# Kernel tuning notes

Measured on AMD Instinct MI355X. Metric: run time of the kernel, lower is better.

## Reference

```python
import jax, jax.numpy as jnp
import numpy as np

T, B, I, H = 512, 64, 1024, 1024


def setup_inputs() -> dict:
    key = jax.random.key(0)
    ks = jax.random.split(key, 7)
    k = 1.0 / np.sqrt(H)  # torch LSTM default init scale
    return {
        "x": jax.random.normal(ks[0], (T, B, I), dtype=jnp.float32),
        "h0": jax.random.normal(ks[1], (B, H), dtype=jnp.float32),
        "c0": jax.random.normal(ks[2], (B, H), dtype=jnp.float32),
        "W_ih": jax.random.uniform(ks[3], (4 * H, I), minval=-k, maxval=k, dtype=jnp.float32),
        "W_hh": jax.random.uniform(ks[4], (4 * H, H), minval=-k, maxval=k, dtype=jnp.float32),
        "b_ih": jax.random.uniform(ks[5], (4 * H,), minval=-k, maxval=k, dtype=jnp.float32),
        "b_hh": jax.random.uniform(ks[6], (4 * H,), minval=-k, maxval=k, dtype=jnp.float32),
    }


def reference(x, h0, c0, W_ih, W_hh, b_ih, b_hh):
    # Precompute input projections for all timesteps in one big GEMM: [T,B,4H]
    x_proj = jnp.einsum("tbi,gi->tbg", x, W_ih) + b_ih

    def step(carry, xg):
        h, c = carry
        gates = xg + h @ W_hh.T + b_hh  # [B, 4H]
        i_g, f_g, g_g, o_g = jnp.split(gates, 4, axis=-1)
        i_g = jax.nn.sigmoid(i_g)
        f_g = jax.nn.sigmoid(f_g)
        g_g = jnp.tanh(g_g)
        o_g = jax.nn.sigmoid(o_g)
        c = f_g * c + i_g * g_g
        h = o_g * jnp.tanh(c)
        return (h, c), h

    (hT, cT), outputs = jax.lax.scan(step, (h0, c0), x_proj)
    return outputs, hT, cT
```

## Files before the change

kernel.cpp:

```cpp
#include <hip/hip_runtime.h>


typedef __attribute__((ext_vector_type(8))) short bf16x8;
typedef __attribute__((ext_vector_type(4))) short bf16x4;
typedef __attribute__((ext_vector_type(4))) float f32x4;
typedef __attribute__((ext_vector_type(4))) unsigned int u32x4;
typedef unsigned long long u64;

#define T_STEPS 512
#define BATCH   64
#define HID     1024
#define G4      4096
#define BH      (BATCH * HID)
#define NSLOT   64

#define OFF_XPT   ((size_t)0)
#define OFF_RING  ((size_t)268435456)
#define OFF_WIB   ((size_t)335544320)
#define OFF_WHB   ((size_t)343932928)
#define OFF_BSUM  ((size_t)352321536)

__device__ __forceinline__ unsigned short f2bf(float f) {
  unsigned int u = __float_as_uint(f);
  u += 0x7FFFu + ((u >> 16) & 1u);
  return (unsigned short)(u >> 16);
}
__device__ __forceinline__ float bf2f(short s) {
  return __uint_as_float(((unsigned int)(unsigned short)s) << 16);
}
__device__ __forceinline__ float sigm(float x) { return 1.0f / (1.0f + __expf(-x)); }
__device__ __forceinline__ float tanh_f(float x) {
  float e = __expf(-2.0f * fabsf(x));
  float r = (1.0f - e) / (1.0f + e);
  return x < 0.0f ? -r : r;
}

__device__ __forceinline__ void gl_lds16(const unsigned short* g, unsigned short* l) {
  __builtin_amdgcn_global_load_lds(
      (const __attribute__((address_space(1))) unsigned int*)g,
      (__attribute__((address_space(3))) unsigned int*)l, 16, 0, 0);
}

__device__ __forceinline__ u32x4 llc_load4(const unsigned int* p) {
  u32x4 r;
  asm volatile("global_load_dwordx4 %0, %1, off sc0 sc1"
               : "=&v"(r) : "v"(p));
  return r;
}

__global__ void k_cast_bf16(const float* __restrict__ src,
                            unsigned short* __restrict__ dst, int n) {
  int i = (blockIdx.x * 256 + threadIdx.x) * 4;
  if (i >= n) return;
  float4 v = *(const float4*)(src + i);
  bf16x4 o;
  o[0] = (short)f2bf(v.x); o[1] = (short)f2bf(v.y);
  o[2] = (short)f2bf(v.z); o[3] = (short)f2bf(v.w);
  *(bf16x4*)(dst + i) = o;
}

__global__ void k_bias(const float* __restrict__ bi, const float* __restrict__ bh,
                       float* __restrict__ bs) {
  int i = blockIdx.x * 256 + threadIdx.x;
  if (i < G4) bs[i] = bi[i] + bh[i];
}

__global__ void k_h0_pack(const float* __restrict__ h0,
                          unsigned int* __restrict__ ring32) {
  int i = blockIdx.x * 256 + threadIdx.x;
  unsigned int pk = ((unsigned int)f2bf(h0[i]) << 16) | 1u;
  __hip_atomic_store(ring32 + i, pk, __ATOMIC_RELAXED, __HIP_MEMORY_SCOPE_AGENT);
}

__launch_bounds__(256, 2)
__global__ void k_xproj(const unsigned short* __restrict__ xb,
                        const unsigned short* __restrict__ wib,
                        const float* __restrict__ bs,
                        unsigned short* __restrict__ xpT) {
  __shared__ __align__(16) unsigned short ldsW[2][128 * 64];
  __shared__ __align__(16) unsigned short ldsX[2][128 * 64];

  const int tid  = threadIdx.x;
  const int lane = tid & 63;
  const int w    = tid >> 6;
  const int nt   = blockIdx.x & 31;
  const int mt   = blockIdx.x >> 5;
  const int n0   = nt * 128;
  const int m0   = mt * 128;
  const int col  = lane & 15;
  const int kq   = lane >> 4;

  const int srow = lane >> 3;
  const int swzu = (lane & 7) ^ srow;

  const unsigned short* wsrc = wib + (size_t)n0 * 1024;
  const unsigned short* xsrc = xb  + (size_t)m0 * 1024;

  const int wm = (w & 1) * 64;
  const int wn = (w >> 1) * 64;

  f32x4 acc[4][4];
#pragma unroll
  for (int i = 0; i < 4; ++i)
#pragma unroll
    for (int j = 0; j < 4; ++j) acc[i][j] = (f32x4){0.f, 0.f, 0.f, 0.f};

  auto STAGE = [&](int b, int kt) {
#pragma unroll
    for (int q = 0; q < 4; ++q) {
      const int rbase = q * 32 + w * 8;
      const size_t goff = (size_t)(rbase + srow) * 1024 + kt * 64 + swzu * 8;
      gl_lds16(wsrc + goff, &ldsW[b][rbase * 64]);
      gl_lds16(xsrc + goff, &ldsX[b][rbase * 64]);
    }
  };

  STAGE(0, 0);
  int buf = 0;
  for (int kt = 0; kt < 16; ++kt) {
    asm volatile("s_waitcnt vmcnt(0)" ::: "memory");
    __syncthreads();
    if (kt < 15) STAGE(buf ^ 1, kt + 1);
#pragma unroll
    for (int ks = 0; ks < 2; ++ks) {
      bf16x8 af[4], bfr[4];
#pragma unroll
      for (int mm = 0; mm < 4; ++mm) {
        const int row = wm + mm * 16 + col;
        const int un  = (ks * 4 + kq) ^ (row & 7);
        af[mm] = *(const bf16x8*)&ldsX[buf][row * 64 + un * 8];
      }
#pragma unroll
      for (int nn = 0; nn < 4; ++nn) {
        const int row = wn + nn * 16 + col;
        const int un  = (ks * 4 + kq) ^ (row & 7);
        bfr[nn] = *(const bf16x8*)&ldsW[buf][row * 64 + un * 8];
      }
#pragma unroll
      for (int mm = 0; mm < 4; ++mm)
#pragma unroll
        for (int nn = 0; nn < 4; ++nn)
          acc[mm][nn] = __builtin_amdgcn_mfma_f32_16x16x32_bf16(
              af[mm], bfr[nn], acc[mm][nn], 0, 0, 0);
    }
    __syncthreads();
    buf ^= 1;
  }

#pragma unroll
  for (int nn = 0; nn < 4; ++nn) {
    const int nrow = n0 + wn + nn * 16 + col;
    const float bias = bs[nrow];
#pragma unroll
    for (int mm = 0; mm < 4; ++mm) {
      bf16x4 ov;
#pragma unroll
      for (int r = 0; r < 4; ++r) ov[r] = (short)f2bf(acc[mm][nn][r] + bias);
      *(bf16x4*)(xpT + (size_t)nrow * 32768 + m0 + wm + mm * 16 + kq * 4) = ov;
    }
  }
}

__launch_bounds__(256, 1)
__global__ void k_lstm(const unsigned short* __restrict__ whb,
                       const unsigned short* __restrict__ xpT,
                       const float* __restrict__ c0,
                       unsigned int* __restrict__ ring32,
                       float* __restrict__ out) {
  const int tid  = threadIdx.x;
  const int lane = tid & 63;
  const int w    = tid >> 6;
  const int jsl  = blockIdx.x & 63;
  const int brow = blockIdx.x >> 6;
  const int b0   = brow * 16;
  const int j0   = jsl * 16;
  const int col  = lane & 15;
  const int kq   = lane >> 4;
  const int kch  = kq * 8;

  __shared__ __align__(16) unsigned char hbf[32 * 1024];
  __shared__ float glds[4][16][17];

  bf16x8 Wr[32];
  {
    const unsigned short* wp = whb + (size_t)(w * 1024 + j0 + col) * 1024 + kch;
#pragma unroll
    for (int s = 0; s < 32; ++s) Wr[s] = *(const bf16x8*)(wp + s * 32);
  }

  const int bl = tid >> 4, cc = tid & 15;
  float c = c0[(b0 + bl) * 1024 + j0 + cc];

  const unsigned short* xprow =
      xpT + (size_t)(w * 1024 + j0 + col) * 32768 + b0 + kq * 4;
  bf16x4 xv = *(const bf16x4*)(xprow);

  const size_t lrow = (size_t)(b0 + col) * 1024 + kq * 8;

  auto STAGE_H = [&](size_t slotbase, unsigned int tg) {
    const unsigned int* sb = ring32 + slotbase + lrow;
    u32x4 q0[8], q1[8];
#pragma unroll
    for (int i = 0; i < 8; ++i) {
      q0[i] = *(const u32x4*)(sb + (w * 8 + i) * 32);
      q1[i] = *(const u32x4*)(sb + (w * 8 + i) * 32 + 4);
    }
    unsigned int pend = 0xFFu;
    for (;;) {
#pragma unroll
      for (int i = 0; i < 8; ++i)
        if (pend & (1u << i)) {
          unsigned int bad =
              ((q0[i][0] ^ tg) | (q0[i][1] ^ tg) | (q0[i][2] ^ tg) | (q0[i][3] ^ tg) |
               (q1[i][0] ^ tg) | (q1[i][1] ^ tg) | (q1[i][2] ^ tg) | (q1[i][3] ^ tg)) &
              0xFFFFu;
          if (bad == 0u) {
            u32x4 o;
            o[0] = (q0[i][0] >> 16) | (q0[i][1] & 0xFFFF0000u);
            o[1] = (q0[i][2] >> 16) | (q0[i][3] & 0xFFFF0000u);
            o[2] = (q1[i][0] >> 16) | (q1[i][1] & 0xFFFF0000u);
            o[3] = (q1[i][2] >> 16) | (q1[i][3] & 0xFFFF0000u);
            *(u32x4*)(hbf + (w * 8 + i) * 1024 + lane * 16) = o;
            pend &= ~(1u << i);
          }
        }
      if (__all(pend == 0u)) break;
#pragma unroll
      for (int i = 0; i < 8; ++i)
        if (pend & (1u << i)) {
          q0[i] = llc_load4(sb + (w * 8 + i) * 32);
          q1[i] = llc_load4(sb + (w * 8 + i) * 32 + 4);
        }
      asm volatile("s_waitcnt vmcnt(0)" ::: "memory");
      __builtin_amdgcn_sched_barrier(0);
    }
  };

  STAGE_H(0, 1u);

  for (int t = 0; t < T_STEPS; ++t) {
    __syncthreads();

    f32x4 acc0 = (f32x4){0.f, 0.f, 0.f, 0.f};
    f32x4 acc1 = (f32x4){0.f, 0.f, 0.f, 0.f};
#pragma unroll
    for (int s = 0; s < 32; s += 2) {
      bf16x8 a0 = *(const bf16x8*)(hbf + s * 1024 + lane * 16);
      bf16x8 a1 = *(const bf16x8*)(hbf + (s + 1) * 1024 + lane * 16);
      acc0 = __builtin_amdgcn_mfma_f32_16x16x32_bf16(a0, Wr[s],     acc0, 0, 0, 0);
      acc1 = __builtin_amdgcn_mfma_f32_16x16x32_bf16(a1, Wr[s + 1], acc1, 0, 0, 0);
    }

#pragma unroll
    for (int r = 0; r < 4; ++r) {
      float v = (acc0[r] + acc1[r]) + bf2f(xv[r]);
      float g = (w == 2) ? tanh_f(v) : sigm(v);
      glds[w][kq * 4 + r][col] = g;
    }
    __syncthreads();

    float ig = glds[0][bl][cc], fg = glds[1][bl][cc];
    float gg = glds[2][bl][cc], og = glds[3][bl][cc];
    c = fg * c + ig * gg;
    float h = og * tanh_f(c);

    if (t < T_STEPS - 1) {
      unsigned int pk = ((unsigned int)f2bf(h) << 16) | (unsigned int)(t + 2);
      __hip_atomic_store(ring32 + (size_t)((t + 1) & (NSLOT - 1)) * BH +
                             (size_t)(b0 + bl) * 1024 + (j0 + cc),
                         pk, __ATOMIC_RELAXED, __HIP_MEMORY_SCOPE_AGENT);
    }

    const int hoff = (b0 + bl) * 1024 + j0 + cc;
    out[(size_t)t * BH + hoff] = h;
    if (t == T_STEPS - 1) {
      out[(size_t)T_STEPS * BH + hoff] = h;
      out[(size_t)T_STEPS * BH + BH + hoff] = c;
    } else {
      xv = *(const bf16x4*)(xprow + (size_t)(t + 1) * 64);
      STAGE_H((size_t)((t + 1) & (NSLOT - 1)) * BH, (unsigned int)(t + 2));
    }
  }
}

extern "C" void kernel_launch(void* const* d_in, const int* in_sizes, int n_in,
                              void* d_out, int out_size, void* d_ws, size_t ws_size,
                              hipStream_t stream) {
  const float* x   = (const float*)d_in[0];
  const float* h0  = (const float*)d_in[1];
  const float* c0  = (const float*)d_in[2];
  const float* Wih = (const float*)d_in[3];
  const float* Whh = (const float*)d_in[4];
  const float* bih = (const float*)d_in[5];
  const float* bhh = (const float*)d_in[6];
  float* out = (float*)d_out;
  char* ws = (char*)d_ws;

  unsigned short* xpT  = (unsigned short*)(ws + OFF_XPT);
  unsigned int*   ring = (unsigned int*)(ws + OFF_RING);
  unsigned short* wib  = (unsigned short*)(ws + OFF_WIB);
  unsigned short* whb  = (unsigned short*)(ws + OFF_WHB);
  float*          bsum = (float*)(ws + OFF_BSUM);

  unsigned short* xb = (unsigned short*)d_out;

  hipMemsetAsync(ring, 0, (size_t)NSLOT * BH * sizeof(unsigned int), stream);

  k_cast_bf16<<<dim3(32768), dim3(256), 0, stream>>>(x, xb, T_STEPS * BATCH * HID);
  k_cast_bf16<<<dim3(4096),  dim3(256), 0, stream>>>(Wih, wib, G4 * HID);
  k_cast_bf16<<<dim3(4096),  dim3(256), 0, stream>>>(Whh, whb, G4 * HID);
  k_h0_pack<<<dim3(256),     dim3(256), 0, stream>>>(h0, ring);
  k_bias<<<dim3(16), dim3(256), 0, stream>>>(bih, bhh, bsum);

  k_xproj<<<dim3(8192), dim3(256), 0, stream>>>(xb, wib, bsum, xpT);
  k_lstm<<<dim3(256), dim3(256), 0, stream>>>(whb, xpT, c0, ring, out);
}
```

Measured before the change: 3.214 ms.

## Fuse input projection into persistent LSTM kernel with pipelined x staging

Removes the separate input-projection GEMM kernel and computes each step's x·W_ih contribution inside the recurrent kernel. W_ih slices are kept in registers next to W_hh, and x tiles for future steps are staged into LDS ahead of time. The intent is to hide this extra MFMA work in the latency-bound recurrence, which spends much of each step waiting on other blocks, and to avoid writing and reading the large x-projection intermediate. In exchange it doubles the weight registers per thread and adds 64KB of LDS and extra MFMA work on the serial critical path.

After: 2.925 ms. 9.0% less time.

```diff
diff --git a/kernel.cpp b/kernel.cpp
--- a/kernel.cpp
+++ b/kernel.cpp
@@ -14,7 +14,7 @@
 #define BH      (BATCH * HID)
 #define NSLOT   64
 
-#define OFF_XPT   ((size_t)0)
+#define OFF_XB    ((size_t)0)
 #define OFF_RING  ((size_t)268435456)
 #define OFF_WIB   ((size_t)335544320)
 #define OFF_WHB   ((size_t)343932928)
@@ -24,9 +24,6 @@
   unsigned int u = __float_as_uint(f);
   u += 0x7FFFu + ((u >> 16) & 1u);
   return (unsigned short)(u >> 16);
-}
-__device__ __forceinline__ float bf2f(short s) {
-  return __uint_as_float(((unsigned int)(unsigned short)s) << 16);
 }
 __device__ __forceinline__ float sigm(float x) { return 1.0f / (1.0f + __expf(-x)); }
 __device__ __forceinline__ float tanh_f(float x) {
@@ -72,98 +69,11 @@
   __hip_atomic_store(ring32 + i, pk, __ATOMIC_RELAXED, __HIP_MEMORY_SCOPE_AGENT);
 }
 
-__launch_bounds__(256, 2)
-__global__ void k_xproj(const unsigned short* __restrict__ xb,
-                        const unsigned short* __restrict__ wib,
-                        const float* __restrict__ bs,
-                        unsigned short* __restrict__ xpT) {
-  __shared__ __align__(16) unsigned short ldsW[2][128 * 64];
-  __shared__ __align__(16) unsigned short ldsX[2][128 * 64];
-
-  const int tid  = threadIdx.x;
-  const int lane = tid & 63;
-  const int w    = tid >> 6;
-  const int nt   = blockIdx.x & 31;
-  const int mt   = blockIdx.x >> 5;
-  const int n0   = nt * 128;
-  const int m0   = mt * 128;
-  const int col  = lane & 15;
-  const int kq   = lane >> 4;
-
-  const int srow = lane >> 3;
-  const int swzu = (lane & 7) ^ srow;
-
-  const unsigned short* wsrc = wib + (size_t)n0 * 1024;
-  const unsigned short* xsrc = xb  + (size_t)m0 * 1024;
-
-  const int wm = (w & 1) * 64;
-  const int wn = (w >> 1) * 64;
-
-  f32x4 acc[4][4];
-#pragma unroll
-  for (int i = 0; i < 4; ++i)
-#pragma unroll
-    for (int j = 0; j < 4; ++j) acc[i][j] = (f32x4){0.f, 0.f, 0.f, 0.f};
-
-  auto STAGE = [&](int b, int kt) {
-#pragma unroll
-    for (int q = 0; q < 4; ++q) {
-      const int rbase = q * 32 + w * 8;
-      const size_t goff = (size_t)(rbase + srow) * 1024 + kt * 64 + swzu * 8;
-      gl_lds16(wsrc + goff, &ldsW[b][rbase * 64]);
-      gl_lds16(xsrc + goff, &ldsX[b][rbase * 64]);
-    }
-  };
-
-  STAGE(0, 0);
-  int buf = 0;
-  for (int kt = 0; kt < 16; ++kt) {
-    asm volatile("s_waitcnt vmcnt(0)" ::: "memory");
-    __syncthreads();
-    if (kt < 15) STAGE(buf ^ 1, kt + 1);
-#pragma unroll
-    for (int ks = 0; ks < 2; ++ks) {
-      bf16x8 af[4], bfr[4];
-#pragma unroll
-      for (int mm = 0; mm < 4; ++mm) {
-        const int row = wm + mm * 16 + col;
-        const int un  = (ks * 4 + kq) ^ (row & 7);
-        af[mm] = *(const bf16x8*)&ldsX[buf][row * 64 + un * 8];
-      }
-#pragma unroll
-      for (int nn = 0; nn < 4; ++nn) {
-        const int row = wn + nn * 16 + col;
-        const int un  = (ks * 4 + kq) ^ (row & 7);
-        bfr[nn] = *(const bf16x8*)&ldsW[buf][row * 64 + un * 8];
-      }
-#pragma unroll
-      for (int mm = 0; mm < 4; ++mm)
-#pragma unroll
-        for (int nn = 0; nn < 4; ++nn)
-          acc[mm][nn] = __builtin_amdgcn_mfma_f32_16x16x32_bf16(
-              af[mm], bfr[nn], acc[mm][nn], 0, 0, 0);
-    }
-    __syncthreads();
-    buf ^= 1;
-  }
-
-#pragma unroll
-  for (int nn = 0; nn < 4; ++nn) {
-    const int nrow = n0 + wn + nn * 16 + col;
-    const float bias = bs[nrow];
-#pragma unroll
-    for (int mm = 0; mm < 4; ++mm) {
-      bf16x4 ov;
-#pragma unroll
-      for (int r = 0; r < 4; ++r) ov[r] = (short)f2bf(acc[mm][nn][r] + bias);
-      *(bf16x4*)(xpT + (size_t)nrow * 32768 + m0 + wm + mm * 16 + kq * 4) = ov;
-    }
-  }
-}
-
 __launch_bounds__(256, 1)
 __global__ void k_lstm(const unsigned short* __restrict__ whb,
-                       const unsigned short* __restrict__ xpT,
+                       const unsigned short* __restrict__ wib,
+                       const unsigned short* __restrict__ xb,
+                       const float* __restrict__ bs,
                        const float* __restrict__ c0,
                        unsigned int* __restrict__ ring32,
                        float* __restrict__ out) {
@@ -179,21 +89,23 @@
   const int kch  = kq * 8;
 
   __shared__ __align__(16) unsigned char hbf[32 * 1024];
+  __shared__ __align__(16) unsigned char xlds[2][32 * 1024];
   __shared__ float glds[4][16][17];
 
-  bf16x8 Wr[32];
+  bf16x8 Wh[32], Wi[32];
   {
-    const unsigned short* wp = whb + (size_t)(w * 1024 + j0 + col) * 1024 + kch;
-#pragma unroll
-    for (int s = 0; s < 32; ++s) Wr[s] = *(const bf16x8*)(wp + s * 32);
+    const unsigned short* wph = whb + (size_t)(w * 1024 + j0 + col) * 1024 + kch;
+    const unsigned short* wpi = wib + (size_t)(w * 1024 + j0 + col) * 1024 + kch;
+#pragma unroll
+    for (int s = 0; s < 32; ++s) {
+      Wh[s] = *(const bf16x8*)(wph + s * 32);
+      Wi[s] = *(const bf16x8*)(wpi + s * 32);
+    }
   }
+  const float bias = bs[w * 1024 + j0 + col];
 
   const int bl = tid >> 4, cc = tid & 15;
   float c = c0[(b0 + bl) * 1024 + j0 + cc];
-
-  const unsigned short* xprow =
-      xpT + (size_t)(w * 1024 + j0 + col) * 32768 + b0 + kq * 4;
-  bf16x4 xv = *(const bf16x4*)(xprow);
 
   const size_t lrow = (size_t)(b0 + col) * 1024 + kq * 8;
 
@@ -236,7 +148,39 @@
     }
   };
 
+  auto STAGE_X = [&](int t_, int slot) {
+    const unsigned short* xs = xb + ((size_t)t_ * 64 + b0 + col) * 1024 + kch;
+#pragma unroll
+    for (int i = 0; i < 8; ++i) {
+      const int s = w * 8 + i;
+      gl_lds16(xs + s * 32, (unsigned short*)(xlds[slot] + s * 1024));
+    }
+  };
+
+  auto XPROJ = [&](int slot) -> f32x4 {
+    f32x4 a0 = (f32x4){0.f, 0.f, 0.f, 0.f};
+    f32x4 a1 = (f32x4){0.f, 0.f, 0.f, 0.f};
+#pragma unroll
+    for (int s = 0; s < 32; s += 2) {
+      bf16x8 x0 = *(const bf16x8*)(xlds[slot] + s * 1024 + lane * 16);
+      bf16x8 x1 = *(const bf16x8*)(xlds[slot] + (s + 1) * 1024 + lane * 16);
+      a0 = __builtin_amdgcn_mfma_f32_16x16x32_bf16(x0, Wi[s],     a0, 0, 0, 0);
+      a1 = __builtin_amdgcn_mfma_f32_16x16x32_bf16(x1, Wi[s + 1], a1, 0, 0, 0);
+    }
+    return a0 + a1;
+  };
+
   STAGE_H(0, 1u);
+  STAGE_X(0, 0);
+  STAGE_X(1, 1);
+  asm volatile("s_waitcnt vmcnt(0)" ::: "memory");
+  __syncthreads();
+  f32x4 xv_cur = XPROJ(0);
+  f32x4 xv_nxt = XPROJ(1);
+  asm volatile("s_waitcnt lgkmcnt(0)" ::: "memory");
+  __builtin_amdgcn_sched_barrier(0);
+  STAGE_X(2, 0);
+  STAGE_X(3, 1);
 
   for (int t = 0; t < T_STEPS; ++t) {
     __syncthreads();
@@ -247,13 +191,13 @@
     for (int s = 0; s < 32; s += 2) {
       bf16x8 a0 = *(const bf16x8*)(hbf + s * 1024 + lane * 16);
       bf16x8 a1 = *(const bf16x8*)(hbf + (s + 1) * 1024 + lane * 16);
-      acc0 = __builtin_amdgcn_mfma_f32_16x16x32_bf16(a0, Wr[s],     acc0, 0, 0, 0);
-      acc1 = __builtin_amdgcn_mfma_f32_16x16x32_bf16(a1, Wr[s + 1], acc1, 0, 0, 0);
+      acc0 = __builtin_amdgcn_mfma_f32_16x16x32_bf16(a0, Wh[s],     acc0, 0, 0, 0);
+      acc1 = __builtin_amdgcn_mfma_f32_16x16x32_bf16(a1, Wh[s + 1], acc1, 0, 0, 0);
     }
 
 #pragma unroll
     for (int r = 0; r < 4; ++r) {
-      float v = (acc0[r] + acc1[r]) + bf2f(xv[r]);
+      float v = (acc0[r] + acc1[r]) + xv_cur[r] + bias;
       float g = (w == 2) ? tanh_f(v) : sigm(v);
       glds[w][kq * 4 + r][col] = g;
     }
@@ -277,8 +221,16 @@
       out[(size_t)T_STEPS * BH + hoff] = h;
       out[(size_t)T_STEPS * BH + BH + hoff] = c;
     } else {
-      xv = *(const bf16x4*)(xprow + (size_t)(t + 1) * 64);
+      f32x4 xnew = xv_nxt;
+      if (t < T_STEPS - 2) xnew = XPROJ(t & 1);
+      xv_cur = xv_nxt;
+      xv_nxt = xnew;
+
       STAGE_H((size_t)((t + 1) & (NSLOT - 1)) * BH, (unsigned int)(t + 2));
+
+      asm volatile("s_waitcnt lgkmcnt(0)" ::: "memory");
+      __builtin_amdgcn_sched_barrier(0);
+      if (t < T_STEPS - 4) STAGE_X(t + 4, t & 1);
     }
   }
 }
@@ -296,22 +248,19 @@
   float* out = (float*)d_out;
   char* ws = (char*)d_ws;
 
-  unsigned short* xpT  = (unsigned short*)(ws + OFF_XPT);
+  unsigned short* xbuf = (unsigned short*)(ws + OFF_XB);
   unsigned int*   ring = (unsigned int*)(ws + OFF_RING);
   unsigned short* wib  = (unsigned short*)(ws + OFF_WIB);
   unsigned short* whb  = (unsigned short*)(ws + OFF_WHB);
   float*          bsum = (float*)(ws + OFF_BSUM);
 
-  unsigned short* xb = (unsigned short*)d_out;
-
   hipMemsetAsync(ring, 0, (size_t)NSLOT * BH * sizeof(unsigned int), stream);
 
-  k_cast_bf16<<<dim3(32768), dim3(256), 0, stream>>>(x, xb, T_STEPS * BATCH * HID);
+  k_cast_bf16<<<dim3(32768), dim3(256), 0, stream>>>(x, xbuf, T_STEPS * BATCH * HID);
   k_cast_bf16<<<dim3(4096),  dim3(256), 0, stream>>>(Wih, wib, G4 * HID);
   k_cast_bf16<<<dim3(4096),  dim3(256), 0, stream>>>(Whh, whb, G4 * HID);
   k_h0_pack<<<dim3(256),     dim3(256), 0, stream>>>(h0, ring);
   k_bias<<<dim3(16), dim3(256), 0, stream>>>(bih, bhh, bsum);
 
-  k_xproj<<<dim3(8192), dim3(256), 0, stream>>>(xb, wib, bsum, xpT);
-  k_lstm<<<dim3(256), dim3(256), 0, stream>>>(whb, xpT, c0, ring, out);
-}
+  k_lstm<<<dim3(256), dim3(256), 0, stream>>>(whb, wib, xbuf, bsum, c0, ring, out);
+}
```
